# Kernel tuning notes

Hardware: AMD Instinct MI355X
Metric: run time of the kernel (lower is better)

Reference implementation:

```python
import jax, jax.numpy as jnp
import numpy as np

N_NODES = 100000
N_EDGES = 1600000
EMB = 128


def setup_inputs() -> dict:
    key = jax.random.key(0)
    k1, k2, k3, k4, k5, k6 = jax.random.split(key, 6)
    embeddings = jax.random.normal(k1, (N_NODES, EMB), dtype=jnp.float32)
    edge_row = jax.random.randint(k2, (N_EDGES,), 0, N_NODES, dtype=jnp.int32)
    edge_col = jax.random.randint(k3, (N_EDGES,), 0, N_NODES, dtype=jnp.int32)
    edge_val = jax.random.uniform(k4, (N_EDGES,), dtype=jnp.float32)
    W1 = jax.random.normal(k5, (EMB, EMB), dtype=jnp.float32) * (1.0 / np.sqrt(EMB))
    W2 = jax.random.normal(k6, (EMB, EMB), dtype=jnp.float32) * (1.0 / np.sqrt(EMB))
    return {"embeddings": embeddings, "edge_row": edge_row, "edge_col": edge_col,
            "edge_val": edge_val, "W1": W1, "W2": W2}


def reference(embeddings, edge_row, edge_col, edge_val, W1, W2):
    # SpMM: relevant = A @ embeddings, A in COO form (row, col, val), shape [N, N]
    gathered = embeddings[edge_col] * edge_val[:, None]          # [E, D]
    relevant = jax.ops.segment_sum(gathered, edge_row, num_segments=N_NODES)  # [N, D]
    # non-interactive + interactive messages
    non_interactive = relevant @ W1                               # [N, D]
    interactive = (relevant * embeddings) @ W2                    # [N, D]
    return non_interactive + interactive
```

## Files before the change

### kernel.cpp

```cpp
#include <hip/hip_runtime.h>
#include <hip/hip_bf16.h>
#include <stdint.h>

#define NN 100000
#define NE 1600000
#define DD 128
#define NBLK 98
#define NBKT 16
#define RPB 6250
#define NCHK 16
#define PBLK 512
#define PTHR 256
#define PCHUNK 3125
#define SEGCAP 288
#define PREPBLK 6266

typedef __attribute__((ext_vector_type(8))) short short8;
typedef __attribute__((ext_vector_type(4))) float f32x4;

__device__ inline unsigned bf16bits(float x) {
  __hip_bfloat16 h = __float2bfloat16(x);
  return (unsigned)*reinterpret_cast<unsigned short*>(&h);
}

__device__ inline float bfhi(unsigned u) { return __uint_as_float(u & 0xffff0000u); }
__device__ inline float bflo(unsigned u) { return __uint_as_float(u << 16); }

__global__ __launch_bounds__(256) void k_front(
    const int* __restrict__ row, const int* __restrict__ col,
    const float* __restrict__ val, uint2* __restrict__ ebuf,
    int* __restrict__ bcnt, const float* __restrict__ emb,
    uint4* __restrict__ tbl, const float* __restrict__ W1,
    const float* __restrict__ W2, uint4* __restrict__ wpack) {
  const int t = threadIdx.x;
  if (blockIdx.x < PBLK) {
    __shared__ int lcnt[NBKT];
    if (t < NBKT) lcnt[t] = 0;
    __syncthreads();
    const int e0 = blockIdx.x * PCHUNK;
    const size_t segbase = (size_t)blockIdx.x * NBKT * SEGCAP;
#pragma unroll 2
    for (int base = 0; base < PCHUNK; base += PTHR) {
      int off = base + t;
      if (off < PCHUNK) {
        int i = e0 + off;
        int r = row[i];
        int m = r / RPB;
        uint2 e;
        e.x = ((unsigned)col[i] << 15) | (bf16bits(val[i]) & 0x7fffu);
        e.y = (unsigned)r;
        int idx = atomicAdd(&lcnt[m], 1);
        if (idx < SEGCAP) ebuf[segbase + (size_t)m * SEGCAP + idx] = e;
      }
    }
    __syncthreads();
    if (t < NBKT) bcnt[blockIdx.x * NBKT + t] = min(lcnt[t], SEGCAP);
  } else if (blockIdx.x < PBLK + 6250) {
    int gid = (blockIdx.x - PBLK) * 256 + t;
    const float4 a = ((const float4*)emb)[2 * gid];
    const float4 b = ((const float4*)emb)[2 * gid + 1];
    uint4 u;
    u.x = bf16bits(a.x) | (bf16bits(a.y) << 16);
    u.y = bf16bits(a.z) | (bf16bits(a.w) << 16);
    u.z = bf16bits(b.x) | (bf16bits(b.y) << 16);
    u.w = bf16bits(b.z) | (bf16bits(b.w) << 16);
    tbl[gid] = u;
  } else {
    int cid = (blockIdx.x - PBLK - 6250) * 256 + t;
    int lane = cid & 63, ct = (cid >> 6) & 7, ks = cid >> 9;
    int colc = ct * 16 + (lane & 15);
    int k0 = ks * 32 + (lane >> 4) * 8;
    unsigned h[8];
#pragma unroll
    for (int j = 0; j < 8; ++j) {
      int kk = k0 + j;
      float w = (kk < DD) ? W1[kk * DD + colc] : W2[(kk - DD) * DD + colc];
      h[j] = bf16bits(w);
    }
    uint4 u;
    u.x = h[0] | (h[1] << 16);
    u.y = h[2] | (h[3] << 16);
    u.z = h[4] | (h[5] << 16);
    u.w = h[6] | (h[7] << 16);
    wpack[cid] = u;
  }
}

__global__ __launch_bounds__(1024) void k_hist(const uint2* __restrict__ ebuf,
                                               const int* __restrict__ bcnt,
                                               int* __restrict__ partial) {
  __shared__ int h[RPB];
  const int m = blockIdx.x & 15, c = blockIdx.x >> 4;
  for (int i = threadIdx.x; i < RPB; i += 1024) h[i] = 0;
  __syncthreads();
  const int base = m * RPB;
  for (int b = c * 32; b < c * 32 + 32; ++b) {
    int scnt = bcnt[b * NBKT + m];
    const uint2* src = ebuf + ((size_t)b * NBKT + m) * SEGCAP;
    for (int i = threadIdx.x; i < scnt; i += 1024)
      atomicAdd(&h[(int)src[i].y - base], 1);
  }
  __syncthreads();
  int* dst = partial + (m * NCHK + c) * RPB;
  for (int i = threadIdx.x; i < RPB; i += 1024) dst[i] = h[i];
}

__global__ __launch_bounds__(1024) void k_scan1(int* __restrict__ partial,
                                                int* __restrict__ offsets,
                                                int* __restrict__ bsum) {
  __shared__ int wsum[16];
  const int t = threadIdx.x, lane = t & 63, wid = t >> 6;
  int i = blockIdx.x * 1024 + t;
  int v = 0;
  if (i < NN) {
    int m = i / RPB, rl = i - m * RPB;
    int* p = partial + (m * NCHK) * RPB + rl;
    int s = 0;
#pragma unroll
    for (int cc = 0; cc < NCHK; ++cc) {
      int x = p[cc * RPB];
      p[cc * RPB] = s;
      s += x;
    }
    v = s;
  }
  int incl = v;
#pragma unroll
  for (int d = 1; d < 64; d <<= 1) {
    int u = __shfl_up(incl, d, 64);
    if (lane >= d) incl += u;
  }
  if (lane == 63) wsum[wid] = incl;
  __syncthreads();
  if (wid == 0) {
    int w = (lane < 16) ? wsum[lane] : 0;
#pragma unroll
    for (int d = 1; d < 16; d <<= 1) {
      int u = __shfl_up(w, d, 64);
      if (lane >= d) w += u;
    }
    if (lane < 16) wsum[lane] = w;
  }
  __syncthreads();
  int wbase = wid ? wsum[wid - 1] : 0;
  if (i < NN) offsets[i] = wbase + incl - v;
  if (t == 0) bsum[blockIdx.x] = wsum[15];
}

__global__ void k_scan2(const int* __restrict__ bsum, int* __restrict__ bpre) {
  const int lane = threadIdx.x;
  int a = bsum[lane];
  int b = (lane + 64 < NBLK) ? bsum[lane + 64] : 0;
  int sa = a, sb = b;
#pragma unroll
  for (int d = 1; d < 64; d <<= 1) {
    int u = __shfl_up(sa, d, 64);
    if (lane >= d) sa += u;
    u = __shfl_up(sb, d, 64);
    if (lane >= d) sb += u;
  }
  int totA = __shfl(sa, 63, 64);
  bpre[lane] = sa - a;
  if (lane + 64 < NBLK) bpre[lane + 64] = totA + sb - b;
}

__global__ __launch_bounds__(1024) void k_scatter3(
    const uint2* __restrict__ ebuf, const int* __restrict__ bcnt,
    const int* __restrict__ partial, const int* __restrict__ offsets,
    const int* __restrict__ bpre, unsigned* __restrict__ cpack) {
  __shared__ int cur[RPB];
  const int m = blockIdx.x & 15, c = blockIdx.x >> 4;
  const int base = m * RPB;
  const int* pre = partial + (m * NCHK + c) * RPB;
  for (int i = threadIdx.x; i < RPB; i += 1024) {
    int r = base + i;
    cur[i] = offsets[r] + bpre[r >> 10] + pre[i];
  }
  __syncthreads();
  for (int b = c * 32; b < c * 32 + 32; ++b) {
    int scnt = bcnt[b * NBKT + m];
    const uint2* src = ebuf + ((size_t)b * NBKT + m) * SEGCAP;
    for (int i = threadIdx.x; i < scnt; i += 1024) {
      uint2 e = src[i];
      int pos = atomicAdd(&cur[(int)e.y - base], 1);
      cpack[pos] = e.x;
    }
  }
}

#define CONSUME(U, W)                                          \
  {                                                            \
    float v = __uint_as_float(((U) << 16) & 0x7fff0000u);      \
    a0 = fmaf(v, bflo((W).x), a0);                             \
    a1 = fmaf(v, bfhi((W).x), a1);                             \
    a2 = fmaf(v, bflo((W).y), a2);                             \
    a3 = fmaf(v, bfhi((W).y), a3);                             \
    a4 = fmaf(v, bflo((W).z), a4);                             \
    a5 = fmaf(v, bfhi((W).z), a5);                             \
    a6 = fmaf(v, bflo((W).w), a6);                             \
    a7 = fmaf(v, bfhi((W).w), a7);                             \
  }

__global__ __launch_bounds__(256) void k_spmm(
    const int* __restrict__ offsets, const int* __restrict__ bpre,
    const unsigned* __restrict__ cpack, const unsigned short* __restrict__ tbl,
    uint4* __restrict__ rel) {
  const int lane = threadIdx.x & 63;
  const int node = blockIdx.x * 4 + (threadIdx.x >> 6);
  if (node >= NN) return;
  const int beg = offsets[node] + bpre[node >> 10];
  const int end = (node + 1 == NN) ? NE : offsets[node + 1] + bpre[(node + 1) >> 10];
  const int q = lane >> 4;
  const int sub = lane & 15;
  const unsigned short* tsub = tbl + (sub << 3);
  float a0 = 0.f, a1 = 0.f, a2 = 0.f, a3 = 0.f;
  float a4 = 0.f, a5 = 0.f, a6 = 0.f, a7 = 0.f;
  for (int j0 = beg; j0 < end; j0 += 64) {
    int idx = j0 + lane;
    unsigned pk = (idx < end) ? cpack[idx] : 0u;
    int n8 = (min(end - j0, 64) + 7) & ~7;
    unsigned uA0 = (unsigned)__shfl((int)pk, q, 64);
    unsigned uA1 = (unsigned)__shfl((int)pk, 4 + q, 64);
    uint4 wA0 = *(const uint4*)(tsub + ((size_t)(uA0 >> 15) << 7));
    uint4 wA1 = *(const uint4*)(tsub + ((size_t)(uA1 >> 15) << 7));
    for (int t = 8; t < n8; t += 8) {
      unsigned uB0 = (unsigned)__shfl((int)pk, t + q, 64);
      unsigned uB1 = (unsigned)__shfl((int)pk, t + 4 + q, 64);
      uint4 wB0 = *(const uint4*)(tsub + ((size_t)(uB0 >> 15) << 7));
      uint4 wB1 = *(const uint4*)(tsub + ((size_t)(uB1 >> 15) << 7));
      CONSUME(uA0, wA0);
      CONSUME(uA1, wA1);
      uA0 = uB0; wA0 = wB0; uA1 = uB1; wA1 = wB1;
    }
    CONSUME(uA0, wA0);
    CONSUME(uA1, wA1);
  }
  a0 += __shfl_xor(a0, 16, 64); a1 += __shfl_xor(a1, 16, 64);
  a2 += __shfl_xor(a2, 16, 64); a3 += __shfl_xor(a3, 16, 64);
  a4 += __shfl_xor(a4, 16, 64); a5 += __shfl_xor(a5, 16, 64);
  a6 += __shfl_xor(a6, 16, 64); a7 += __shfl_xor(a7, 16, 64);
  a0 += __shfl_xor(a0, 32, 64); a1 += __shfl_xor(a1, 32, 64);
  a2 += __shfl_xor(a2, 32, 64); a3 += __shfl_xor(a3, 32, 64);
  a4 += __shfl_xor(a4, 32, 64); a5 += __shfl_xor(a5, 32, 64);
  a6 += __shfl_xor(a6, 32, 64); a7 += __shfl_xor(a7, 32, 64);
  if (lane < 16) {
    uint4 o;
    o.x = bf16bits(a0) | (bf16bits(a1) << 16);
    o.y = bf16bits(a2) | (bf16bits(a3) << 16);
    o.z = bf16bits(a4) | (bf16bits(a5) << 16);
    o.w = bf16bits(a6) | (bf16bits(a7) << 16);
    rel[(size_t)node * 16 + sub] = o;
  }
}

__device__ inline short8 bfmul8(short8 a, short8 b) {
  short8 r;
#pragma unroll
  for (int i = 0; i < 8; ++i) {
    float fa = __uint_as_float(((unsigned)(unsigned short)a[i]) << 16);
    float fb = __uint_as_float(((unsigned)(unsigned short)b[i]) << 16);
    r[i] = (short)bf16bits(fa * fb);
  }
  return r;
}

__global__ __launch_bounds__(256) void k_phase2(
    const unsigned short* __restrict__ rel, const unsigned short* __restrict__ tbl,
    const uint4* __restrict__ wpack, float* __restrict__ out) {
  __shared__ uint4 bw[4096];
  for (int i = threadIdx.x; i < 4096; i += 256) bw[i] = wpack[i];
  __syncthreads();

  const int lane = threadIdx.x & 63;
  const int wid = threadIdx.x >> 6;
  const long Rw = (long)blockIdx.x * 128 + wid * 32;

  long r0 = Rw + (lane & 15);
  long r1 = r0 + 16;
  if (r0 >= NN) r0 = NN - 1;
  if (r1 >= NN) r1 = NN - 1;
  const int fo = (lane >> 4) * 8;

  f32x4 acc[2][8] = {};

#pragma unroll
  for (int ks = 0; ks < 4; ++ks) {
    short8 rf0 = *(const short8*)(rel + r0 * DD + ks * 32 + fo);
    short8 ef0 = *(const short8*)(tbl + r0 * DD + ks * 32 + fo);
    short8 rf1 = *(const short8*)(rel + r1 * DD + ks * 32 + fo);
    short8 ef1 = *(const short8*)(tbl + r1 * DD + ks * 32 + fo);
    short8 m0 = bfmul8(rf0, ef0);
    short8 m1 = bfmul8(rf1, ef1);
#pragma unroll
    for (int ct = 0; ct < 8; ++ct) {
      short8 b1 = *(const short8*)&bw[(ks * 8 + ct) * 64 + lane];
      short8 b2 = *(const short8*)&bw[((ks + 4) * 8 + ct) * 64 + lane];
      acc[0][ct] = __builtin_amdgcn_mfma_f32_16x16x32_bf16(rf0, b1, acc[0][ct], 0, 0, 0);
      acc[0][ct] = __builtin_amdgcn_mfma_f32_16x16x32_bf16(m0, b2, acc[0][ct], 0, 0, 0);
      acc[1][ct] = __builtin_amdgcn_mfma_f32_16x16x32_bf16(rf1, b1, acc[1][ct], 0, 0, 0);
      acc[1][ct] = __builtin_amdgcn_mfma_f32_16x16x32_bf16(m1, b2, acc[1][ct], 0, 0, 0);
    }
  }

  const int orow = (lane >> 4) * 4;
  const int ocol = lane & 15;
#pragma unroll
  for (int rt = 0; rt < 2; ++rt) {
    long rbase = Rw + rt * 16 + orow;
#pragma unroll
    for (int ct = 0; ct < 8; ++ct) {
#pragma unroll
      for (int qq = 0; qq < 4; ++qq) {
        long rr = rbase + qq;
        if (rr < NN) out[rr * DD + ct * 16 + ocol] = acc[rt][ct][qq];
      }
    }
  }
}

extern "C" void kernel_launch(void* const* d_in, const int* in_sizes, int n_in,
                              void* d_out, int out_size, void* d_ws, size_t ws_size,
                              hipStream_t stream) {
  const float* emb = (const float*)d_in[0];
  const int* erow = (const int*)d_in[1];
  const int* ecol = (const int*)d_in[2];
  const float* eva = (const float*)d_in[3];
  const float* W1 = (const float*)d_in[4];
  const float* W2 = (const float*)d_in[5];
  float* out = (float*)d_out;

  char* ws = (char*)d_ws;
  unsigned short* tbl = (unsigned short*)(ws);
  unsigned short* rel = (unsigned short*)(ws + 25600000);
  uint2* ebuf = (uint2*)(ws + 25600000);
  int* partial = (int*)(ws + 25600000 + 18874368);
  int* bcnt = (int*)(ws + 25600000 + 25274368);
  int* offsets = (int*)(ws + 51200000);
  unsigned* cpack = (unsigned*)(ws + 52000128);
  int* bsum = (int*)(ws + 58400128);
  int* bpre = (int*)(ws + 58400640);
  uint4* wpack = (uint4*)(ws + 58401152);

  k_front<<<PBLK + PREPBLK, 256, 0, stream>>>(erow, ecol, eva, ebuf, bcnt,
                                              emb, (uint4*)tbl, W1, W2, wpack);
  k_hist<<<NBKT * NCHK, 1024, 0, stream>>>(ebuf, bcnt, partial);
  k_scan1<<<NBLK, 1024, 0, stream>>>(partial, offsets, bsum);
  k_scan2<<<1, 64, 0, stream>>>(bsum, bpre);
  k_scatter3<<<NBKT * NCHK, 1024, 0, stream>>>(ebuf, bcnt, partial, offsets, bpre, cpack);
  k_spmm<<<NN / 4, 256, 0, stream>>>(offsets, bpre, cpack, tbl, (uint4*)rel);
  k_phase2<<<(NN + 127) / 128, 256, 0, stream>>>(rel, tbl, wpack, out);
}
```

Baseline: 142.5 us.

## Fuse SpMM and dense projection into one kernel via shared-memory staging

Merges the SpMM kernel and the MFMA projection kernel into one. Each 512-thread block aggregates 32 rows and writes both relevant and relevant*emb as bf16 into XOR-swizzled shared memory. It then runs the 32x256x128 MFMA GEMM from LDS, with weights read directly from global memory. This removes the intermediate rel round trip through HBM and one kernel launch, at the cost of per-block synchronisation, lower occupancy, and weight reloads per block instead of an LDS-cached copy.

```diff
diff --git a/kernel.cpp b/kernel.cpp
--- a/kernel.cpp
+++ b/kernel.cpp
@@ -201,120 +201,92 @@
     a7 = fmaf(v, bfhi((W).w), a7);                             \
   }
 
-__global__ __launch_bounds__(256) void k_spmm(
+__global__ __launch_bounds__(512) void k_fused(
     const int* __restrict__ offsets, const int* __restrict__ bpre,
     const unsigned* __restrict__ cpack, const unsigned short* __restrict__ tbl,
-    uint4* __restrict__ rel) {
+    const uint4* __restrict__ wpack, float* __restrict__ out) {
+  __shared__ short As[32 * 256];
   const int lane = threadIdx.x & 63;
-  const int node = blockIdx.x * 4 + (threadIdx.x >> 6);
-  if (node >= NN) return;
-  const int beg = offsets[node] + bpre[node >> 10];
-  const int end = (node + 1 == NN) ? NE : offsets[node + 1] + bpre[(node + 1) >> 10];
-  const int q = lane >> 4;
+  const int wid = threadIdx.x >> 6;
+  const int q4 = lane >> 4;
   const int sub = lane & 15;
   const unsigned short* tsub = tbl + (sub << 3);
-  float a0 = 0.f, a1 = 0.f, a2 = 0.f, a3 = 0.f;
-  float a4 = 0.f, a5 = 0.f, a6 = 0.f, a7 = 0.f;
-  for (int j0 = beg; j0 < end; j0 += 64) {
-    int idx = j0 + lane;
-    unsigned pk = (idx < end) ? cpack[idx] : 0u;
-    int n8 = (min(end - j0, 64) + 7) & ~7;
-    unsigned uA0 = (unsigned)__shfl((int)pk, q, 64);
-    unsigned uA1 = (unsigned)__shfl((int)pk, 4 + q, 64);
-    uint4 wA0 = *(const uint4*)(tsub + ((size_t)(uA0 >> 15) << 7));
-    uint4 wA1 = *(const uint4*)(tsub + ((size_t)(uA1 >> 15) << 7));
-    for (int t = 8; t < n8; t += 8) {
-      unsigned uB0 = (unsigned)__shfl((int)pk, t + q, 64);
-      unsigned uB1 = (unsigned)__shfl((int)pk, t + 4 + q, 64);
-      uint4 wB0 = *(const uint4*)(tsub + ((size_t)(uB0 >> 15) << 7));
-      uint4 wB1 = *(const uint4*)(tsub + ((size_t)(uB1 >> 15) << 7));
+
+  for (int j = 0; j < 4; ++j) {
+    const int r = wid * 4 + j;
+    const int node = blockIdx.x * 32 + r;
+    const int beg = offsets[node] + bpre[node >> 10];
+    const int end = (node + 1 == NN) ? NE : offsets[node + 1] + bpre[(node + 1) >> 10];
+    float a0 = 0.f, a1 = 0.f, a2 = 0.f, a3 = 0.f;
+    float a4 = 0.f, a5 = 0.f, a6 = 0.f, a7 = 0.f;
+    for (int j0 = beg; j0 < end; j0 += 64) {
+      int idx = j0 + lane;
+      unsigned pk = (idx < end) ? cpack[idx] : 0u;
+      int n8 = (min(end - j0, 64) + 7) & ~7;
+      unsigned uA0 = (unsigned)__shfl((int)pk, q4, 64);
+      unsigned uA1 = (unsigned)__shfl((int)pk, 4 + q4, 64);
+      uint4 wA0 = *(const uint4*)(tsub + ((size_t)(uA0 >> 15) << 7));
+      uint4 wA1 = *(const uint4*)(tsub + ((size_t)(uA1 >> 15) << 7));
+      for (int t = 8; t < n8; t += 8) {
+        unsigned uB0 = (unsigned)__shfl((int)pk, t + q4, 64);
+        unsigned uB1 = (unsigned)__shfl((int)pk, t + 4 + q4, 64);
+        uint4 wB0 = *(const uint4*)(tsub + ((size_t)(uB0 >> 15) << 7));
+        uint4 wB1 = *(const uint4*)(tsub + ((size_t)(uB1 >> 15) << 7));
+        CONSUME(uA0, wA0);
+        CONSUME(uA1, wA1);
+        uA0 = uB0; wA0 = wB0; uA1 = uB1; wA1 = wB1;
+      }
       CONSUME(uA0, wA0);
       CONSUME(uA1, wA1);
-      uA0 = uB0; wA0 = wB0; uA1 = uB1; wA1 = wB1;
-    }
-    CONSUME(uA0, wA0);
-    CONSUME(uA1, wA1);
-  }
-  a0 += __shfl_xor(a0, 16, 64); a1 += __shfl_xor(a1, 16, 64);
-  a2 += __shfl_xor(a2, 16, 64); a3 += __shfl_xor(a3, 16, 64);
-  a4 += __shfl_xor(a4, 16, 64); a5 += __shfl_xor(a5, 16, 64);
-  a6 += __shfl_xor(a6, 16, 64); a7 += __shfl_xor(a7, 16, 64);
-  a0 += __shfl_xor(a0, 32, 64); a1 += __shfl_xor(a1, 32, 64);
-  a2 += __shfl_xor(a2, 32, 64); a3 += __shfl_xor(a3, 32, 64);
-  a4 += __shfl_xor(a4, 32, 64); a5 += __shfl_xor(a5, 32, 64);
-  a6 += __shfl_xor(a6, 32, 64); a7 += __shfl_xor(a7, 32, 64);
-  if (lane < 16) {
-    uint4 o;
-    o.x = bf16bits(a0) | (bf16bits(a1) << 16);
-    o.y = bf16bits(a2) | (bf16bits(a3) << 16);
-    o.z = bf16bits(a4) | (bf16bits(a5) << 16);
-    o.w = bf16bits(a6) | (bf16bits(a7) << 16);
-    rel[(size_t)node * 16 + sub] = o;
-  }
-}
-
-__device__ inline short8 bfmul8(short8 a, short8 b) {
-  short8 r;
-#pragma unroll
-  for (int i = 0; i < 8; ++i) {
-    float fa = __uint_as_float(((unsigned)(unsigned short)a[i]) << 16);
-    float fb = __uint_as_float(((unsigned)(unsigned short)b[i]) << 16);
-    r[i] = (short)bf16bits(fa * fb);
-  }
-  return r;
-}
-
-__global__ __launch_bounds__(256) void k_phase2(
-    const unsigned short* __restrict__ rel, const unsigned short* __restrict__ tbl,
-    const uint4* __restrict__ wpack, float* __restrict__ out) {
-  __shared__ uint4 bw[4096];
-  for (int i = threadIdx.x; i < 4096; i += 256) bw[i] = wpack[i];
-  __syncthreads();
-
-  const int lane = threadIdx.x & 63;
-  const int wid = threadIdx.x >> 6;
-  const long Rw = (long)blockIdx.x * 128 + wid * 32;
-
-  long r0 = Rw + (lane & 15);
-  long r1 = r0 + 16;
-  if (r0 >= NN) r0 = NN - 1;
-  if (r1 >= NN) r1 = NN - 1;
-  const int fo = (lane >> 4) * 8;
-
-  f32x4 acc[2][8] = {};
-
-#pragma unroll
-  for (int ks = 0; ks < 4; ++ks) {
-    short8 rf0 = *(const short8*)(rel + r0 * DD + ks * 32 + fo);
-    short8 ef0 = *(const short8*)(tbl + r0 * DD + ks * 32 + fo);
-    short8 rf1 = *(const short8*)(rel + r1 * DD + ks * 32 + fo);
-    short8 ef1 = *(const short8*)(tbl + r1 * DD + ks * 32 + fo);
-    short8 m0 = bfmul8(rf0, ef0);
-    short8 m1 = bfmul8(rf1, ef1);
-#pragma unroll
-    for (int ct = 0; ct < 8; ++ct) {
-      short8 b1 = *(const short8*)&bw[(ks * 8 + ct) * 64 + lane];
-      short8 b2 = *(const short8*)&bw[((ks + 4) * 8 + ct) * 64 + lane];
-      acc[0][ct] = __builtin_amdgcn_mfma_f32_16x16x32_bf16(rf0, b1, acc[0][ct], 0, 0, 0);
-      acc[0][ct] = __builtin_amdgcn_mfma_f32_16x16x32_bf16(m0, b2, acc[0][ct], 0, 0, 0);
-      acc[1][ct] = __builtin_amdgcn_mfma_f32_16x16x32_bf16(rf1, b1, acc[1][ct], 0, 0, 0);
-      acc[1][ct] = __builtin_amdgcn_mfma_f32_16x16x32_bf16(m1, b2, acc[1][ct], 0, 0, 0);
-    }
-  }
-
-  const int orow = (lane >> 4) * 4;
-  const int ocol = lane & 15;
-#pragma unroll
-  for (int rt = 0; rt < 2; ++rt) {
-    long rbase = Rw + rt * 16 + orow;
-#pragma unroll
-    for (int ct = 0; ct < 8; ++ct) {
-#pragma unroll
-      for (int qq = 0; qq < 4; ++qq) {
-        long rr = rbase + qq;
-        if (rr < NN) out[rr * DD + ct * 16 + ocol] = acc[rt][ct][qq];
-      }
-    }
+    }
+    a0 += __shfl_xor(a0, 16, 64); a1 += __shfl_xor(a1, 16, 64);
+    a2 += __shfl_xor(a2, 16, 64); a3 += __shfl_xor(a3, 16, 64);
+    a4 += __shfl_xor(a4, 16, 64); a5 += __shfl_xor(a5, 16, 64);
+    a6 += __shfl_xor(a6, 16, 64); a7 += __shfl_xor(a7, 16, 64);
+    a0 += __shfl_xor(a0, 32, 64); a1 += __shfl_xor(a1, 32, 64);
+    a2 += __shfl_xor(a2, 32, 64); a3 += __shfl_xor(a3, 32, 64);
+    a4 += __shfl_xor(a4, 32, 64); a5 += __shfl_xor(a5, 32, 64);
+    a6 += __shfl_xor(a6, 32, 64); a7 += __shfl_xor(a7, 32, 64);
+    if (q4 == 0) {
+      uint4 o;
+      o.x = bf16bits(a0) | (bf16bits(a1) << 16);
+      o.y = bf16bits(a2) | (bf16bits(a3) << 16);
+      o.z = bf16bits(a4) | (bf16bits(a5) << 16);
+      o.w = bf16bits(a6) | (bf16bits(a7) << 16);
+      *(uint4*)(As + r * 256 + ((sub ^ (r & 7)) << 3)) = o;
+    } else if (q4 == 1) {
+      uint4 tw = *(const uint4*)(tbl + (size_t)node * DD + (sub << 3));
+      uint4 om;
+      om.x = bf16bits(a0 * bflo(tw.x)) | (bf16bits(a1 * bfhi(tw.x)) << 16);
+      om.y = bf16bits(a2 * bflo(tw.y)) | (bf16bits(a3 * bfhi(tw.y)) << 16);
+      om.z = bf16bits(a4 * bflo(tw.z)) | (bf16bits(a5 * bfhi(tw.z)) << 16);
+      om.w = bf16bits(a6 * bflo(tw.w)) | (bf16bits(a7 * bfhi(tw.w)) << 16);
+      *(uint4*)(As + r * 256 + (((16 + sub) ^ (r & 7)) << 3)) = om;
+    }
+  }
+  __syncthreads();
+
+  const int ct = wid;
+  f32x4 acc0 = {0.f, 0.f, 0.f, 0.f};
+  f32x4 acc1 = {0.f, 0.f, 0.f, 0.f};
+#pragma unroll
+  for (int ks = 0; ks < 8; ++ks) {
+    const int slot = ks * 4 + q4;
+    const int r0 = sub;
+    const int r1 = sub + 16;
+    short8 aT = *(const short8*)(As + r0 * 256 + ((slot ^ (r0 & 7)) << 3));
+    short8 aB = *(const short8*)(As + r1 * 256 + ((slot ^ (r1 & 7)) << 3));
+    short8 b = *(const short8*)(wpack + (size_t)(ks * 8 + ct) * 64 + lane);
+    acc0 = __builtin_amdgcn_mfma_f32_16x16x32_bf16(aT, b, acc0, 0, 0, 0);
+    acc1 = __builtin_amdgcn_mfma_f32_16x16x32_bf16(aB, b, acc1, 0, 0, 0);
+  }
+  const long Rb = (long)blockIdx.x * 32;
+  const int ocol = ct * 16 + sub;
+  const int orow = q4 * 4;
+#pragma unroll
+  for (int qq = 0; qq < 4; ++qq) {
+    out[(Rb + orow + qq) * DD + ocol] = acc0[qq];
+    out[(Rb + 16 + orow + qq) * DD + ocol] = acc1[qq];
   }
 }
 
@@ -331,7 +303,6 @@
 
   char* ws = (char*)d_ws;
   unsigned short* tbl = (unsigned short*)(ws);
-  unsigned short* rel = (unsigned short*)(ws + 25600000);
   uint2* ebuf = (uint2*)(ws + 25600000);
   int* partial = (int*)(ws + 25600000 + 18874368);
   int* bcnt = (int*)(ws + 25600000 + 25274368);
@@ -347,6 +318,5 @@
   k_scan1<<<NBLK, 1024, 0, stream>>>(partial, offsets, bsum);
   k_scan2<<<1, 64, 0, stream>>>(bsum, bpre);
   k_scatter3<<<NBKT * NCHK, 1024, 0, stream>>>(ebuf, bcnt, partial, offsets, bpre, cpack);
-  k_spmm<<<NN / 4, 256, 0, stream>>>(offsets, bpre, cpack, tbl, (uint4*)rel);
-  k_phase2<<<(NN + 127) / 128, 256, 0, stream>>>(rel, tbl, wpack, out);
-}
+  k_fused<<<NN / 32, 512, 0, stream>>>(offsets, bpre, cpack, tbl, wpack, out);
+}
```

Result: faster. 131.5 us (-7.7%).
